# Performance work log

Hardware: AMD Instinct MI355X
Metric: run time of the kernel (lower is better)

The kernel has to match this reference:

```python
import math
import jax, jax.numpy as jnp
import numpy as np

DIM = 192
HEADS = 6
HD = DIM // HEADS          # 32
WS = (2, 8, 8)             # window_size (D, H, W)
NUM = WS[0] * WS[1] * WS[2]  # 128 tokens per window
SCALE = HD ** -0.5
BATCH = 1024               # number of windows (B * nW)
NW = 64                    # windows per shift-mask group


def _rel_index():
    # replicates WindowAttention.get_position_index
    coords = np.stack(np.meshgrid(*[np.arange(w) for w in WS], indexing='ij')).reshape(3, -1)
    rel = coords[:, :, None] - coords[:, None, :]          # [3, N, N]
    rel = rel.transpose(1, 2, 0).copy()                    # [N, N, 3]
    for i in range(3):
        rel[:, :, i] += WS[i] - 1
    rel[:, :, 0] *= (2 * WS[1] - 1) * (2 * WS[2] - 1)
    rel[:, :, 1] *= 2 * WS[2] - 1
    return rel.sum(-1).astype(np.int32)                    # [N, N]


def _sine_pos(H, W, feat):
    # replicates get_sine_position_encoding(size=(H,W), num_position_features=feat, normalize=True)
    eps = 1e-6
    scale = 2 * math.pi
    temp = 10000.0
    y = np.broadcast_to(np.arange(1, H + 1, dtype=np.float32)[:, None], (H, W))
    x = np.broadcast_to(np.arange(1, W + 1, dtype=np.float32)[None, :], (H, W))
    y = y / (H + eps) * scale
    x = x / (W + eps) * scale
    dim_t = temp ** (2 * (np.arange(feat, dtype=np.float32) // 2) / feat)  # [feat]
    def enc(e):
        p = e[:, :, None] / dim_t                          # [H, W, feat]
        return np.stack([np.sin(p[:, :, 0::2]), np.cos(p[:, :, 1::2])], axis=3).reshape(H, W, feat)
    pos = np.concatenate([enc(y), enc(x)], axis=2)         # [H, W, 2*feat]
    return pos.reshape(1, H * W, 2 * feat).astype(np.float32)  # [1, H*W, dim]


def setup_inputs() -> dict:
    key = jax.random.key(0)
    ks = jax.random.split(key, 8)
    x = jax.random.normal(ks[0], (BATCH, NUM, DIM), dtype=jnp.float32)
    mask = jax.random.normal(ks[1], (NW, NUM, NUM), dtype=jnp.float32)
    w_qkv = jax.random.normal(ks[2], (DIM, 3 * DIM), dtype=jnp.float32) * 0.02
    w_qkv_mutual = jax.random.normal(ks[3], (DIM, 3 * DIM), dtype=jnp.float32) * 0.02
    w_proj = jax.random.normal(ks[4], (2 * DIM, DIM), dtype=jnp.float32) * 0.02
    b_proj = jnp.zeros((DIM,), dtype=jnp.float32)
    n_rel = (2 * WS[0] - 1) * (2 * WS[1] - 1) * (2 * WS[2] - 1)  # 675
    rpb_table = jax.random.normal(ks[5], (n_rel, HEADS), dtype=jnp.float32) * 0.02
    position_bias = jnp.asarray(_sine_pos(WS[1], WS[2], DIM // 2))  # [1, 64, 192]
    rel_pos_index = jnp.asarray(_rel_index())                       # [128, 128] int32
    return {
        'x': x, 'mask': mask, 'w_qkv': w_qkv, 'w_qkv_mutual': w_qkv_mutual,
        'w_proj': w_proj, 'b_proj': b_proj, 'rpb_table': rpb_table,
        'position_bias': position_bias, 'rel_pos_index': rel_pos_index,
    }


def _attention(q, k, v, mask, bias):
    # q,k,v: [B, H, n, d]; mask: [nW, N, N] or None; bias: [1, H, n, n] or None
    B, Hh, n, d = q.shape
    attn = jnp.einsum('bhqd,bhkd->bhqk', q * SCALE, k)
    if bias is not None:
        attn = attn + bias
    if mask is not None:
        nW = mask.shape[0]
        attn = attn.reshape(B // nW, nW, Hh, n, n) + mask[None, :, None, :n, :n]
        attn = attn.reshape(B, Hh, n, n)
    attn = jax.nn.softmax(attn, axis=-1)
    out = jnp.einsum('bhqk,bhkd->bhqd', attn, v)
    return out.transpose(0, 2, 1, 3).reshape(B, n, Hh * d)


def reference(x, mask, w_qkv, w_qkv_mutual, w_proj, b_proj, rpb_table, position_bias, rel_pos_index):
    B, N, C = x.shape
    # self windowed attention with gathered relative position bias
    qkv = (x @ w_qkv).reshape(B, N, 3, HEADS, HD).transpose(2, 0, 3, 1, 4)
    q, k, v = qkv[0], qkv[1], qkv[2]
    bias = rpb_table[rel_pos_index.reshape(-1)].reshape(N, N, HEADS)
    bias = bias.transpose(2, 0, 1)[None]                   # [1, H, N, N]
    out = _attention(q, k, v, mask, bias)                  # [B, N, C]
    # mutual cross-window branch
    pb = jnp.tile(position_bias, (1, 2, 1))                # [1, N, C]
    qkv_m = ((x + pb) @ w_qkv_mutual).reshape(B, N, 3, HEADS, HD).transpose(2, 0, 3, 1, 4)
    qm, km, vm = qkv_m[0], qkv_m[1], qkv_m[2]
    q1, q2 = jnp.split(qm, 2, axis=2)
    k1, k2 = jnp.split(km, 2, axis=2)
    v1, v2 = jnp.split(vm, 2, axis=2)
    aligned0 = _attention(q2, k1, v1, mask, None)          # [B, N/2, C]
    aligned1 = _attention(q1, k2, v2, mask, None)          # [B, N/2, C]
    out = jnp.concatenate([jnp.concatenate([aligned0, aligned1], axis=1), out], axis=2)  # [B, N, 2C]
    return out @ w_proj + b_proj                           # [B, N, C]
```

## Files before the change

### kernel.cpp

```cpp
#include <hip/hip_runtime.h>
#include <hip/hip_bf16.h>
#include <math.h>


#define SCALE_F 0.17677669529663687f
#define LOG2E_F 1.4426950408889634f

#define WS_WQKV_T   0u
#define WS_WQKVM_T  221184u
#define WS_WPROJ_T  442368u
#define WS_RPBG     589824u
#define WS_NEEDED   786432u

typedef __bf16 bf16x8 __attribute__((ext_vector_type(8)));
typedef __bf16 bf16x4 __attribute__((ext_vector_type(4)));
typedef float  f32x4  __attribute__((ext_vector_type(4)));

#define MFMA(a, b, c) __builtin_amdgcn_mfma_f32_16x16x32_bf16((a), (b), (c), 0, 0, 0)

#if __has_builtin(__builtin_amdgcn_exp2f)
#define EXP2(x) __builtin_amdgcn_exp2f(x)
#else
#define EXP2(x) exp2f(x)
#endif
#if __has_builtin(__builtin_amdgcn_rcpf)
#define RCP(x) __builtin_amdgcn_rcpf(x)
#else
#define RCP(x) (1.0f / (x))
#endif

#define GLOAD_LDS(gp, lp)                                                   \
    __builtin_amdgcn_global_load_lds(                                       \
        (const __attribute__((address_space(1))) unsigned int*)(gp),        \
        (__attribute__((address_space(3))) unsigned int*)(lp), 16, 0, 0)

__global__ void prep_kernel(const float* __restrict__ w_qkv,
                            const float* __restrict__ w_qkvm,
                            const float* __restrict__ w_proj,
                            const float* __restrict__ rpb_table,
                            const int*   __restrict__ rel_idx,
                            char* __restrict__ ws) {
    int idx = blockIdx.x * 256 + threadIdx.x;
    if (idx < 110592) {
        int col = idx / 192, k = idx - col * 192;
        float sc = (col < 192) ? SCALE_F * LOG2E_F : 1.0f;
        int dst = (k >> 5) * 18432 + col * 32 + (k & 31);
        ((__bf16*)(ws + WS_WQKV_T))[dst]  = (__bf16)(w_qkv[k * 576 + col] * sc);
        ((__bf16*)(ws + WS_WQKVM_T))[dst] = (__bf16)(w_qkvm[k * 576 + col] * sc);
    } else if (idx < 184320) {
        int o = idx - 110592;
        int n = o / 384, k = o - n * 384;
        ((__bf16*)(ws + WS_WPROJ_T))[o] = (__bf16)w_proj[k * 192 + n];
    } else if (idx < 282624) {
        int o = idx - 184320;
        int h = o / 16384, r2 = o - h * 16384;
        int i = r2 >> 7, c = r2 & 127;
        int half = c >> 6, cc = c & 63;
        int l16 = cc >> 2, jj = cc & 3;
        int jcol = l16 + (half * 4 + jj) * 16;
        ((__bf16*)(ws + WS_RPBG))[o] =
            (__bf16)(rpb_table[rel_idx[i * 128 + jcol] * 6 + h] * LOG2E_F);
    }
}

__global__ __launch_bounds__(512, 4)
void attn_kernel(const float* __restrict__ x,
                 const float* __restrict__ mask,
                 const float* __restrict__ pos_bias,
                 const char*  __restrict__ ws,
                 __bf16* __restrict__ concat) {
    __shared__ alignas(16) __bf16 wbuf[18432];
    __shared__ alignas(16) __bf16 kh1[128][40];
    __shared__ alignas(16) __bf16 vt1[32][136];
    __shared__ alignas(16) __bf16 qs[8][16][72];

    const int i0     = blockIdx.x;
    const int xcd    = i0 & 7;
    const int j0     = i0 >> 3;
    const int branch = j0 & 1;
    const int wm     = (j0 >> 5) * 8 + xcd;
    const int b      = ((j0 >> 1) & 15) * 64 + wm;

    const int tid  = threadIdx.x;
    const int wave = tid >> 6;
    const int lane = tid & 63;
    const int quad = lane >> 4;
    const int l16  = lane & 15;
    const int mrow = wave * 16;

    const __bf16* wt   = (const __bf16*)(ws + (branch ? WS_WQKVM_T : WS_WQKV_T));
    const __bf16* rpbg = (const __bf16*)(ws + WS_RPBG);
    __bf16 (*qw)[72] = qs[wave];

    const int sl8 = (lane ^ ((lane >> 3) & 7)) * 8;
    const int spq = (l16 * 4 + quad);
    const int sp8 = (spq ^ ((spq >> 3) & 7)) * 8;

    auto stage = [&](int h) {
        #pragma unroll
        for (int ii = 0; ii < 5; ++ii) {
            const int i = wave + ii * 8;
            if (i < 36) {
                const int p = i / 12, r = i - p * 12;
                const int ks = r >> 1, half = r & 1;
                const __bf16* gp = wt + ks * 18432
                    + (p * 192 + h * 32 + half * 16) * 32 + sl8;
                GLOAD_LDS(gp, &wbuf[i * 512]);
            }
        }
    };

    bf16x8 afrag[6];
    {
        const float* xr = x + (size_t)b * 24576 + (mrow + l16) * 192;
        const float* pr = pos_bias + ((mrow + l16) & 63) * 192;
        #pragma unroll
        for (int ks = 0; ks < 6; ++ks) {
            const int k0 = ks * 32 + quad * 8;
            float4 v0 = *(const float4*)(xr + k0);
            float4 v1 = *(const float4*)(xr + k0 + 4);
            if (branch) {
                float4 p0 = *(const float4*)(pr + k0);
                float4 p1 = *(const float4*)(pr + k0 + 4);
                v0.x += p0.x; v0.y += p0.y; v0.z += p0.z; v0.w += p0.w;
                v1.x += p1.x; v1.y += p1.y; v1.z += p1.z; v1.w += p1.w;
            }
            bf16x8 f;
            f[0] = (__bf16)v0.x; f[1] = (__bf16)v0.y;
            f[2] = (__bf16)v0.z; f[3] = (__bf16)v0.w;
            f[4] = (__bf16)v1.x; f[5] = (__bf16)v1.y;
            f[6] = (__bf16)v1.z; f[7] = (__bf16)v1.w;
            afrag[ks] = f;
        }
    }

    auto runproj2 = [&](int p, f32x4* acc) {
        const int cb = p * 6144;
        #pragma unroll
        for (int ks = 0; ks < 6; ++ks) {
            bf16x8 b0 = *(const bf16x8*)&wbuf[cb + ks * 1024 + sp8];
            bf16x8 b1 = *(const bf16x8*)&wbuf[cb + ks * 1024 + 512 + sp8];
            acc[0] = MFMA(afrag[ks], b0, acc[0]);
            acc[1] = MFMA(afrag[ks], b1, acc[1]);
        }
    };

    stage(0);
    __syncthreads();

    #pragma unroll 1
    for (int h = 0; h < 6; ++h) {
        {
            f32x4 acc[2] = {};
            runproj2(1, acc);
            #pragma unroll
            for (int nt = 0; nt < 2; ++nt)
                #pragma unroll
                for (int r = 0; r < 4; ++r)
                    kh1[mrow + quad * 4 + r][nt * 16 + l16] = (__bf16)acc[nt][r];
        }
        {
            f32x4 acc[2] = {};
            runproj2(2, acc);
            #pragma unroll
            for (int nt = 0; nt < 2; ++nt) {
                bf16x4 pv;
                #pragma unroll
                for (int r = 0; r < 4; ++r) pv[r] = (__bf16)acc[nt][r];
                *(bf16x4*)&vt1[nt * 16 + l16][mrow + quad * 4] = pv;
            }
        }
        bf16x8 aq;
        {
            f32x4 acc[2] = {};
            runproj2(0, acc);
            #pragma unroll
            for (int nt = 0; nt < 2; ++nt)
                #pragma unroll
                for (int r = 0; r < 4; ++r)
                    qw[quad * 4 + r][nt * 16 + l16] = (__bf16)acc[nt][r];
            aq = *(const bf16x8*)&qw[l16][quad * 8];
        }
        __syncthreads();

        if (h < 5) stage(h + 1);

        f32x4 o0 = {}, o1 = {};
        float rsum[4] = {0.f, 0.f, 0.f, 0.f};

        if (branch == 0) {
            const float*  mp = mask + ((size_t)wm * 128 + mrow + quad * 4) * 128 + l16;
            const __bf16* rb = rpbg + ((size_t)(h * 128 + mrow + quad * 4) << 7) + l16 * 4;
            #pragma unroll
            for (int half = 0; half < 2; ++half) {
                f32x4 s4[4];
                #pragma unroll
                for (int r = 0; r < 4; ++r) {
                    bf16x4 rvr = *(const bf16x4*)(rb + r * 128 + half * 64);
                    #pragma unroll
                    for (int j = 0; j < 4; ++j)
                        s4[j][r] = fmaf(mp[r * 128 + (half * 4 + j) * 16],
                                        LOG2E_F, (float)rvr[j]);
                }
                #pragma unroll
                for (int j = 0; j < 4; ++j) {
                    bf16x8 bk = *(const bf16x8*)
                        &kh1[(half * 4 + j) * 16 + l16][quad * 8];
                    s4[j] = MFMA(aq, bk, s4[j]);
                }
                #pragma unroll
                for (int r = 0; r < 4; ++r)
                    #pragma unroll
                    for (int j = 0; j < 4; ++j) {
                        float p = EXP2(s4[j][r]);
                        s4[j][r] = p;
                        rsum[r] += p;
                    }
                #pragma unroll
                for (int j = 0; j < 4; ++j)
                    #pragma unroll
                    for (int r = 0; r < 4; ++r)
                        qw[quad * 4 + r][j * 16 + l16] = (__bf16)s4[j][r];
                #pragma unroll
                for (int kb = 0; kb < 2; ++kb) {
                    bf16x8 p = *(const bf16x8*)&qw[l16][kb * 32 + quad * 8];
                    bf16x8 bv0 = *(const bf16x8*)
                        &vt1[l16][half * 64 + kb * 32 + quad * 8];
                    bf16x8 bv1 = *(const bf16x8*)
                        &vt1[16 + l16][half * 64 + kb * 32 + quad * 8];
                    o0 = MFMA(p, bv0, o0);
                    o1 = MFMA(p, bv1, o1);
                }
            }
        } else {
            const int kbase = (mrow < 64) ? 64 : 0;
            const float* mp = mask
                + ((size_t)wm * 128 + ((mrow + quad * 4) & 63)) * 128 + l16;
            f32x4 s4[4];
            #pragma unroll
            for (int r = 0; r < 4; ++r)
                #pragma unroll
                for (int j = 0; j < 4; ++j)
                    s4[j][r] = mp[r * 128 + j * 16] * LOG2E_F;
            #pragma unroll
            for (int j = 0; j < 4; ++j) {
                bf16x8 bk = *(const bf16x8*)
                    &kh1[kbase + j * 16 + l16][quad * 8];
                s4[j] = MFMA(aq, bk, s4[j]);
            }
            #pragma unroll
            for (int r = 0; r < 4; ++r)
                #pragma unroll
                for (int j = 0; j < 4; ++j) {
                    float p = EXP2(s4[j][r]);
                    s4[j][r] = p;
                    rsum[r] += p;
                }
            #pragma unroll
            for (int j = 0; j < 4; ++j)
                #pragma unroll
                for (int r = 0; r < 4; ++r)
                    qw[quad * 4 + r][j * 16 + l16] = (__bf16)s4[j][r];
            #pragma unroll
            for (int kb = 0; kb < 2; ++kb) {
                bf16x8 p = *(const bf16x8*)&qw[l16][kb * 32 + quad * 8];
                bf16x8 bv0 = *(const bf16x8*)
                    &vt1[l16][kbase + kb * 32 + quad * 8];
                bf16x8 bv1 = *(const bf16x8*)
                    &vt1[16 + l16][kbase + kb * 32 + quad * 8];
                o0 = MFMA(p, bv0, o0);
                o1 = MFMA(p, bv1, o1);
            }
        }

        float rl[4];
        #pragma unroll
        for (int r = 0; r < 4; ++r) {
            float sum = rsum[r];
            #pragma unroll
            for (int off = 1; off < 16; off <<= 1)
                sum += __shfl_xor(sum, off, 64);
            rl[r] = RCP(sum);
        }
        __syncthreads();

        #pragma unroll
        for (int r = 0; r < 4; ++r) {
            qw[quad * 4 + r][l16]      = (__bf16)(o0[r] * rl[r]);
            qw[quad * 4 + r][16 + l16] = (__bf16)(o1[r] * rl[r]);
        }
        {
            const int rloc = lane >> 2;
            const int cpart = (lane & 3) * 8;
            uint4 val = *(const uint4*)&qw[rloc][cpart];
            const int grow = mrow + rloc;
            const int rowm = branch ? ((grow + 64) & 127) : grow;
            const int colofs = branch ? 0 : 192;
            *(uint4*)&concat[((size_t)b * 128 + rowm) * 384 + colofs + h * 32 + cpart] = val;
        }
    }
}

__global__ __launch_bounds__(512, 4)
void proj_kernel(const __bf16* __restrict__ concat,
                 const char* __restrict__ ws,
                 const float* __restrict__ b_proj,
                 float* __restrict__ out) {
    __shared__ alignas(16) __bf16 bwA[18432];
    __shared__ alignas(16) __bf16 bwB[18432];
    const __bf16* wp = (const __bf16*)(ws + WS_WPROJ_T);
    const int tid  = threadIdx.x;
    const int wave = tid >> 6;
    const int lane = tid & 63;
    const int quad = lane >> 4;
    const int l16  = lane & 15;
    const int mrow = wave * 16;
    const size_t r0 = (size_t)blockIdx.x * 128;

    const int sl8 = (lane ^ ((lane >> 3) & 7)) * 8;

    bf16x8 a[12];
    {
        const __bf16* arow = concat + (r0 + mrow + l16) * 384;
        #pragma unroll
        for (int ks = 0; ks < 12; ++ks)
            a[ks] = *(const bf16x8*)&arow[ks * 32 + quad * 8];
    }

    auto stageP = [&](int c, __bf16* buf) {
        #pragma unroll
        for (int ii = 0; ii < 5; ++ii) {
            const int i = wave + ii * 8;
            if (i < 36) {
                const int e = i * 512 + sl8;
                const int row = e / 96;
                const int col = e - row * 96;
                const __bf16* gp = wp + row * 384 + c * 96 + col;
                GLOAD_LDS(gp, &buf[i * 512]);
            }
        }
    };

    f32x4 acc[12] = {};
    auto computeC = [&](const __bf16* buf, int c) {
        #pragma unroll
        for (int k3 = 0; k3 < 3; ++k3) {
            bf16x8 af = a[c * 3 + k3];
            #pragma unroll
            for (int nt = 0; nt < 12; ++nt) {
                const int s  = l16 * 12 + quad + nt * 192 + k3 * 4;
                const int sp = s ^ ((s >> 3) & 7);
                bf16x8 bb = *(const bf16x8*)&buf[sp * 8];
                acc[nt] = MFMA(af, bb, acc[nt]);
            }
        }
    };

    stageP(0, bwA);
    __syncthreads();
    stageP(1, bwB);
    computeC(bwA, 0);
    __syncthreads();
    stageP(2, bwA);
    computeC(bwB, 1);
    __syncthreads();
    stageP(3, bwB);
    computeC(bwA, 2);
    __syncthreads();
    computeC(bwB, 3);

    #pragma unroll
    for (int nt = 0; nt < 12; ++nt) {
        const int cc = nt * 16 + l16;
        const float bias = b_proj[cc];
        #pragma unroll
        for (int r = 0; r < 4; ++r)
            out[(r0 + mrow + quad * 4 + r) * 192 + cc] = acc[nt][r] + bias;
    }
}

extern "C" void kernel_launch(void* const* d_in, const int* in_sizes, int n_in,
                              void* d_out, int out_size, void* d_ws, size_t ws_size,
                              hipStream_t stream) {
    const float* x       = (const float*)d_in[0];
    const float* mask    = (const float*)d_in[1];
    const float* w_qkv   = (const float*)d_in[2];
    const float* w_qkvm  = (const float*)d_in[3];
    const float* w_proj  = (const float*)d_in[4];
    const float* b_proj  = (const float*)d_in[5];
    const float* rpb     = (const float*)d_in[6];
    const float* pos_b   = (const float*)d_in[7];
    const int*   rel_idx = (const int*)d_in[8];

    if (ws_size < WS_NEEDED) return;

    char*   ws     = (char*)d_ws;
    __bf16* concat = (__bf16*)d_out;
    float*  out    = (float*)d_out;

    prep_kernel<<<1104, 256, 0, stream>>>(w_qkv, w_qkvm, w_proj, rpb, rel_idx, ws);
    attn_kernel<<<2048, 512, 0, stream>>>(x, mask, pos_b, ws, concat);
    proj_kernel<<<1024, 512, 0, stream>>>(concat, ws, b_proj, out);
}
```

Baseline: 395.5 us.

## Fuse attention branches and output projection into one kernel per window

Merges the two-branch attention kernel and the projection kernel into a single kernel where each block processes both the self and mutual branches for one window, then runs the output projection. LDS is shared through a union-style buffer, and the weight staging for the next branch is prefetched at the end of the previous one. This removes a kernel launch and lets the concat intermediate be re-read while it is likely still cached. In exchange, per-window parallelism is halved, since each block now runs both branches serially, and the in-place concat/out aliasing within a block must stay correctly ordered.

```diff
diff --git a/kernel.cpp b/kernel.cpp
--- a/kernel.cpp
+++ b/kernel.cpp
@@ -64,22 +64,25 @@
 }
 
 __global__ __launch_bounds__(512, 4)
-void attn_kernel(const float* __restrict__ x,
-                 const float* __restrict__ mask,
-                 const float* __restrict__ pos_bias,
-                 const char*  __restrict__ ws,
-                 __bf16* __restrict__ concat) {
-    __shared__ alignas(16) __bf16 wbuf[18432];
-    __shared__ alignas(16) __bf16 kh1[128][40];
-    __shared__ alignas(16) __bf16 vt1[32][136];
-    __shared__ alignas(16) __bf16 qs[8][16][72];
-
-    const int i0     = blockIdx.x;
-    const int xcd    = i0 & 7;
-    const int j0     = i0 >> 3;
-    const int branch = j0 & 1;
-    const int wm     = (j0 >> 5) * 8 + xcd;
-    const int b      = ((j0 >> 1) & 15) * 64 + wm;
+void fused_kernel(const float* __restrict__ x,
+                  const float* __restrict__ mask,
+                  const float* __restrict__ pos_bias,
+                  const char*  __restrict__ ws,
+                  const float* __restrict__ b_proj,
+                  float* __restrict__ out) {
+    __shared__ alignas(16) char smem[74240];
+    __bf16* wbuf            = (__bf16*)smem;
+    __bf16 (*kh1)[40]       = (__bf16(*)[40])(smem + 36864);
+    __bf16 (*vt1)[136]      = (__bf16(*)[136])(smem + 47104);
+    __bf16 (*qs)[16][72]    = (__bf16(*)[16][72])(smem + 55808);
+    __bf16* bwA             = (__bf16*)smem;
+    __bf16* bwB             = (__bf16*)(smem + 36864);
+
+    const int i0  = blockIdx.x;
+    const int xcd = i0 & 7;
+    const int j0  = i0 >> 3;
+    const int wm  = (j0 >> 4) * 8 + xcd;
+    const int b   = (j0 & 15) * 64 + wm;
 
     const int tid  = threadIdx.x;
     const int wave = tid >> 6;
@@ -88,22 +91,22 @@
     const int l16  = lane & 15;
     const int mrow = wave * 16;
 
-    const __bf16* wt   = (const __bf16*)(ws + (branch ? WS_WQKVM_T : WS_WQKV_T));
     const __bf16* rpbg = (const __bf16*)(ws + WS_RPBG);
+    __bf16* concat = (__bf16*)out;
     __bf16 (*qw)[72] = qs[wave];
 
     const int sl8 = (lane ^ ((lane >> 3) & 7)) * 8;
-    const int spq = (l16 * 4 + quad);
+    const int spq = l16 * 4 + quad;
     const int sp8 = (spq ^ ((spq >> 3) & 7)) * 8;
 
-    auto stage = [&](int h) {
+    auto stageW = [&](const __bf16* wtb, int h) {
         #pragma unroll
         for (int ii = 0; ii < 5; ++ii) {
             const int i = wave + ii * 8;
             if (i < 36) {
                 const int p = i / 12, r = i - p * 12;
                 const int ks = r >> 1, half = r & 1;
-                const __bf16* gp = wt + ks * 18432
+                const __bf16* gp = wtb + ks * 18432
                     + (p * 192 + h * 32 + half * 16) * 32 + sl8;
                 GLOAD_LDS(gp, &wbuf[i * 512]);
             }
@@ -111,7 +114,7 @@
     };
 
     bf16x8 afrag[6];
-    {
+    auto loadA = [&](int br) {
         const float* xr = x + (size_t)b * 24576 + (mrow + l16) * 192;
         const float* pr = pos_bias + ((mrow + l16) & 63) * 192;
         #pragma unroll
@@ -119,7 +122,7 @@
             const int k0 = ks * 32 + quad * 8;
             float4 v0 = *(const float4*)(xr + k0);
             float4 v1 = *(const float4*)(xr + k0 + 4);
-            if (branch) {
+            if (br) {
                 float4 p0 = *(const float4*)(pr + k0);
                 float4 p1 = *(const float4*)(pr + k0 + 4);
                 v0.x += p0.x; v0.y += p0.y; v0.z += p0.z; v0.w += p0.w;
@@ -132,7 +135,7 @@
             f[6] = (__bf16)v1.z; f[7] = (__bf16)v1.w;
             afrag[ks] = f;
         }
-    }
+    };
 
     auto runproj2 = [&](int p, f32x4* acc) {
         const int cb = p * 6144;
@@ -145,67 +148,116 @@
         }
     };
 
-    stage(0);
+    stageW((const __bf16*)(ws + WS_WQKV_T), 0);
+    loadA(0);
     __syncthreads();
 
     #pragma unroll 1
-    for (int h = 0; h < 6; ++h) {
-        {
-            f32x4 acc[2] = {};
-            runproj2(1, acc);
-            #pragma unroll
-            for (int nt = 0; nt < 2; ++nt)
+    for (int br = 0; br < 2; ++br) {
+        const __bf16* wtb = (const __bf16*)(ws + (br ? WS_WQKVM_T : WS_WQKV_T));
+        if (br) loadA(1);
+        #pragma unroll 1
+        for (int h = 0; h < 6; ++h) {
+            {
+                f32x4 acc[2] = {};
+                runproj2(1, acc);
+                #pragma unroll
+                for (int nt = 0; nt < 2; ++nt)
+                    #pragma unroll
+                    for (int r = 0; r < 4; ++r)
+                        kh1[mrow + quad * 4 + r][nt * 16 + l16] = (__bf16)acc[nt][r];
+            }
+            {
+                f32x4 acc[2] = {};
+                runproj2(2, acc);
+                #pragma unroll
+                for (int nt = 0; nt < 2; ++nt) {
+                    bf16x4 pv;
+                    #pragma unroll
+                    for (int r = 0; r < 4; ++r) pv[r] = (__bf16)acc[nt][r];
+                    *(bf16x4*)&vt1[nt * 16 + l16][mrow + quad * 4] = pv;
+                }
+            }
+            bf16x8 aq;
+            {
+                f32x4 acc[2] = {};
+                runproj2(0, acc);
+                #pragma unroll
+                for (int nt = 0; nt < 2; ++nt)
+                    #pragma unroll
+                    for (int r = 0; r < 4; ++r)
+                        qw[quad * 4 + r][nt * 16 + l16] = (__bf16)acc[nt][r];
+                aq = *(const bf16x8*)&qw[l16][quad * 8];
+            }
+            __syncthreads();
+
+            if (!(br == 1 && h == 5)) {
+                const __bf16* nwt = (h == 5)
+                    ? (const __bf16*)(ws + WS_WQKVM_T) : wtb;
+                stageW(nwt, (h == 5) ? 0 : h + 1);
+            }
+
+            f32x4 o0 = {}, o1 = {};
+            float rsum[4] = {0.f, 0.f, 0.f, 0.f};
+
+            if (br == 0) {
+                const float*  mp = mask + ((size_t)wm * 128 + mrow + quad * 4) * 128 + l16;
+                const __bf16* rb = rpbg + ((size_t)(h * 128 + mrow + quad * 4) << 7) + l16 * 4;
+                #pragma unroll
+                for (int half = 0; half < 2; ++half) {
+                    f32x4 s4[4];
+                    #pragma unroll
+                    for (int r = 0; r < 4; ++r) {
+                        bf16x4 rvr = *(const bf16x4*)(rb + r * 128 + half * 64);
+                        #pragma unroll
+                        for (int j = 0; j < 4; ++j)
+                            s4[j][r] = fmaf(mp[r * 128 + (half * 4 + j) * 16],
+                                            LOG2E_F, (float)rvr[j]);
+                    }
+                    #pragma unroll
+                    for (int j = 0; j < 4; ++j) {
+                        bf16x8 bk = *(const bf16x8*)
+                            &kh1[(half * 4 + j) * 16 + l16][quad * 8];
+                        s4[j] = MFMA(aq, bk, s4[j]);
+                    }
+                    #pragma unroll
+                    for (int r = 0; r < 4; ++r)
+                        #pragma unroll
+                        for (int j = 0; j < 4; ++j) {
+                            float p = EXP2(s4[j][r]);
+                            s4[j][r] = p;
+                            rsum[r] += p;
+                        }
+                    #pragma unroll
+                    for (int j = 0; j < 4; ++j)
+                        #pragma unroll
+                        for (int r = 0; r < 4; ++r)
+                            qw[quad * 4 + r][j * 16 + l16] = (__bf16)s4[j][r];
+                    #pragma unroll
+                    for (int kb = 0; kb < 2; ++kb) {
+                        bf16x8 p = *(const bf16x8*)&qw[l16][kb * 32 + quad * 8];
+                        bf16x8 bv0 = *(const bf16x8*)
+                            &vt1[l16][half * 64 + kb * 32 + quad * 8];
+                        bf16x8 bv1 = *(const bf16x8*)
+                            &vt1[16 + l16][half * 64 + kb * 32 + quad * 8];
+                        o0 = MFMA(p, bv0, o0);
+                        o1 = MFMA(p, bv1, o1);
+                    }
+                }
+            } else {
+                const int kbase = (mrow < 64) ? 64 : 0;
+                const float* mp = mask
+                    + ((size_t)wm * 128 + ((mrow + quad * 4) & 63)) * 128 + l16;
+                f32x4 s4[4];
                 #pragma unroll
                 for (int r = 0; r < 4; ++r)
-                    kh1[mrow + quad * 4 + r][nt * 16 + l16] = (__bf16)acc[nt][r];
-        }
-        {
-            f32x4 acc[2] = {};
-            runproj2(2, acc);
-            #pragma unroll
-            for (int nt = 0; nt < 2; ++nt) {
-                bf16x4 pv;
-                #pragma unroll
-                for (int r = 0; r < 4; ++r) pv[r] = (__bf16)acc[nt][r];
-                *(bf16x4*)&vt1[nt * 16 + l16][mrow + quad * 4] = pv;
-            }
-        }
-        bf16x8 aq;
-        {
-            f32x4 acc[2] = {};
-            runproj2(0, acc);
-            #pragma unroll
-            for (int nt = 0; nt < 2; ++nt)
-                #pragma unroll
-                for (int r = 0; r < 4; ++r)
-                    qw[quad * 4 + r][nt * 16 + l16] = (__bf16)acc[nt][r];
-            aq = *(const bf16x8*)&qw[l16][quad * 8];
-        }
-        __syncthreads();
-
-        if (h < 5) stage(h + 1);
-
-        f32x4 o0 = {}, o1 = {};
-        float rsum[4] = {0.f, 0.f, 0.f, 0.f};
-
-        if (branch == 0) {
-            const float*  mp = mask + ((size_t)wm * 128 + mrow + quad * 4) * 128 + l16;
-            const __bf16* rb = rpbg + ((size_t)(h * 128 + mrow + quad * 4) << 7) + l16 * 4;
-            #pragma unroll
-            for (int half = 0; half < 2; ++half) {
-                f32x4 s4[4];
-                #pragma unroll
-                for (int r = 0; r < 4; ++r) {
-                    bf16x4 rvr = *(const bf16x4*)(rb + r * 128 + half * 64);
                     #pragma unroll
                     for (int j = 0; j < 4; ++j)
-                        s4[j][r] = fmaf(mp[r * 128 + (half * 4 + j) * 16],
-                                        LOG2E_F, (float)rvr[j]);
-                }
+                        s4[j][r] = mp[r * 128 + j * 16] * LOG2E_F;
                 #pragma unroll
                 for (int j = 0; j < 4; ++j) {
                     bf16x8 bk = *(const bf16x8*)
-                        &kh1[(half * 4 + j) * 16 + l16][quad * 8];
+                        &kh1[kbase + j * 16 + l16][quad * 8];
                     s4[j] = MFMA(aq, bk, s4[j]);
                 }
                 #pragma unroll
@@ -225,99 +277,46 @@
                 for (int kb = 0; kb < 2; ++kb) {
                     bf16x8 p = *(const bf16x8*)&qw[l16][kb * 32 + quad * 8];
                     bf16x8 bv0 = *(const bf16x8*)
-                        &vt1[l16][half * 64 + kb * 32 + quad * 8];
+                        &vt1[l16][kbase + kb * 32 + quad * 8];
                     bf16x8 bv1 = *(const bf16x8*)
-                        &vt1[16 + l16][half * 64 + kb * 32 + quad * 8];
+                        &vt1[16 + l16][kbase + kb * 32 + quad * 8];
                     o0 = MFMA(p, bv0, o0);
                     o1 = MFMA(p, bv1, o1);
                 }
             }
-        } else {
-            const int kbase = (mrow < 64) ? 64 : 0;
-            const float* mp = mask
-                + ((size_t)wm * 128 + ((mrow + quad * 4) & 63)) * 128 + l16;
-            f32x4 s4[4];
+
+            float rl[4];
             #pragma unroll
-            for (int r = 0; r < 4; ++r)
-                #pragma unroll
-                for (int j = 0; j < 4; ++j)
-                    s4[j][r] = mp[r * 128 + j * 16] * LOG2E_F;
+            for (int r = 0; r < 4; ++r) {
+                float sum = rsum[r];
+                #pragma unroll
+                for (int off = 1; off < 16; off <<= 1)
+                    sum += __shfl_xor(sum, off, 64);
+                rl[r] = RCP(sum);
+            }
+            __syncthreads();
+
             #pragma unroll
-            for (int j = 0; j < 4; ++j) {
-                bf16x8 bk = *(const bf16x8*)
-                    &kh1[kbase + j * 16 + l16][quad * 8];
-                s4[j] = MFMA(aq, bk, s4[j]);
-            }
-            #pragma unroll
-            for (int r = 0; r < 4; ++r)
-                #pragma unroll
-                for (int j = 0; j < 4; ++j) {
-                    float p = EXP2(s4[j][r]);
-                    s4[j][r] = p;
-                    rsum[r] += p;
-                }
-            #pragma unroll
-            for (int j = 0; j < 4; ++j)
-                #pragma unroll
-                for (int r = 0; r < 4; ++r)
-                    qw[quad * 4 + r][j * 16 + l16] = (__bf16)s4[j][r];
-            #pragma unroll
-            for (int kb = 0; kb < 2; ++kb) {
-                bf16x8 p = *(const bf16x8*)&qw[l16][kb * 32 + quad * 8];
-                bf16x8 bv0 = *(const bf16x8*)
-                    &vt1[l16][kbase + kb * 32 + quad * 8];
-                bf16x8 bv1 = *(const bf16x8*)
-                    &vt1[16 + l16][kbase + kb * 32 + quad * 8];
-                o0 = MFMA(p, bv0, o0);
-                o1 = MFMA(p, bv1, o1);
-            }
-        }
-
-        float rl[4];
-        #pragma unroll
-        for (int r = 0; r < 4; ++r) {
-            float sum = rsum[r];
-            #pragma unroll
-            for (int off = 1; off < 16; off <<= 1)
-                sum += __shfl_xor(sum, off, 64);
-            rl[r] = RCP(sum);
-        }
-        __syncthreads();
-
-        #pragma unroll
-        for (int r = 0; r < 4; ++r) {
-            qw[quad * 4 + r][l16]      = (__bf16)(o0[r] * rl[r]);
-            qw[quad * 4 + r][16 + l16] = (__bf16)(o1[r] * rl[r]);
-        }
-        {
-            const int rloc = lane >> 2;
-            const int cpart = (lane & 3) * 8;
-            uint4 val = *(const uint4*)&qw[rloc][cpart];
-            const int grow = mrow + rloc;
-            const int rowm = branch ? ((grow + 64) & 127) : grow;
-            const int colofs = branch ? 0 : 192;
-            *(uint4*)&concat[((size_t)b * 128 + rowm) * 384 + colofs + h * 32 + cpart] = val;
+            for (int r = 0; r < 4; ++r) {
+                qw[quad * 4 + r][l16]      = (__bf16)(o0[r] * rl[r]);
+                qw[quad * 4 + r][16 + l16] = (__bf16)(o1[r] * rl[r]);
+            }
+            {
+                const int rloc = lane >> 2;
+                const int cpart = (lane & 3) * 8;
+                uint4 val = *(const uint4*)&qw[rloc][cpart];
+                const int grow = mrow + rloc;
+                const int rowm = br ? ((grow + 64) & 127) : grow;
+                const int colofs = br ? 0 : 192;
+                *(uint4*)&concat[((size_t)b * 128 + rowm) * 384 + colofs + h * 32 + cpart] = val;
+            }
         }
     }
-}
-
-__global__ __launch_bounds__(512, 4)
-void proj_kernel(const __bf16* __restrict__ concat,
-                 const char* __restrict__ ws,
-                 const float* __restrict__ b_proj,
-                 float* __restrict__ out) {
-    __shared__ alignas(16) __bf16 bwA[18432];
-    __shared__ alignas(16) __bf16 bwB[18432];
+
+    __syncthreads();
+
     const __bf16* wp = (const __bf16*)(ws + WS_WPROJ_T);
-    const int tid  = threadIdx.x;
-    const int wave = tid >> 6;
-    const int lane = tid & 63;
-    const int quad = lane >> 4;
-    const int l16  = lane & 15;
-    const int mrow = wave * 16;
-    const size_t r0 = (size_t)blockIdx.x * 128;
-
-    const int sl8 = (lane ^ ((lane >> 3) & 7)) * 8;
+    const size_t r0 = (size_t)b * 128;
 
     bf16x8 a[12];
     {
@@ -394,11 +393,9 @@
 
     if (ws_size < WS_NEEDED) return;
 
-    char*   ws     = (char*)d_ws;
-    __bf16* concat = (__bf16*)d_out;
-    float*  out    = (float*)d_out;
+    char*  ws  = (char*)d_ws;
+    float* out = (float*)d_out;
 
     prep_kernel<<<1104, 256, 0, stream>>>(w_qkv, w_qkvm, w_proj, rpb, rel_idx, ws);
-    attn_kernel<<<2048, 512, 0, stream>>>(x, mask, pos_b, ws, concat);
-    proj_kernel<<<1024, 512, 0, stream>>>(concat, ws, b_proj, out);
+    fused_kernel<<<1024, 512, 0, stream>>>(x, mask, pos_b, ws, b_proj, out);
 }
```

After: 386.4 us. -2.3%, faster.
